# Performance work log

Hardware: AMD Instinct MI355X
Metric: run time of the kernel (lower is better)

The kernel has to match this reference:

```python
import jax, jax.numpy as jnp
import numpy as np

N = 100000
F_IN = 128
HIDDEN = 64
HEADS = 4
EPS = 1e-16
SLOPE = 0.2  # PyG GATConv default negative_slope


def gat_conv(x, src, dst, W, a_src, a_dst, b, heads, out_ch, concat, n_nodes):
    # x: [N, F]; W: [F, heads*out_ch]; a_src/a_dst: [heads, out_ch]
    h = (x @ W).reshape(n_nodes, heads, out_ch)              # [N, H, C]
    alpha_s = jnp.einsum('nhc,hc->nh', h, a_src)             # [N, H]
    alpha_d = jnp.einsum('nhc,hc->nh', h, a_dst)             # [N, H]
    e = alpha_s[src] + alpha_d[dst]                          # [E, H]
    e = jnp.where(e > 0, e, SLOPE * e)                       # leaky_relu
    # segment softmax over destination node
    m = jax.ops.segment_max(e, dst, num_segments=n_nodes)    # [N, H]
    m = jnp.where(jnp.isfinite(m), m, 0.0)                   # empty segments
    ex = jnp.exp(e - m[dst])                                 # [E, H]
    denom = jax.ops.segment_sum(ex, dst, num_segments=n_nodes)  # [N, H]
    alpha = ex / (denom[dst] + EPS)                          # [E, H]
    # weighted scatter-aggregate of source features at destinations
    msg = h[src] * alpha[:, :, None]                         # [E, H, C]
    out = jax.ops.segment_sum(msg, dst, num_segments=n_nodes)  # [N, H, C]
    if concat:
        out = out.reshape(n_nodes, heads * out_ch)
    else:
        out = out.mean(axis=1)
    return out + b


def setup_inputs() -> dict:
    key = jax.random.key(0)
    ks = jax.random.split(key, 12)
    x = jax.random.normal(ks[0], (N, F_IN), dtype=jnp.float32)
    edge_index = jax.random.randint(ks[1], (2, 1600000), 0, N, dtype=jnp.int64)
    s1 = 1.0 / np.sqrt(F_IN)
    s2 = 1.0 / np.sqrt(HIDDEN)
    return {
        'x': x,
        'edge_index': edge_index,
        'W1': jax.random.normal(ks[2], (F_IN, HIDDEN), dtype=jnp.float32) * s1,
        'a_src1': jax.random.normal(ks[3], (HEADS, HIDDEN // HEADS), dtype=jnp.float32) * s2,
        'a_dst1': jax.random.normal(ks[4], (HEADS, HIDDEN // HEADS), dtype=jnp.float32) * s2,
        'b1': jnp.zeros((HIDDEN,), dtype=jnp.float32),
        'W2': jax.random.normal(ks[5], (HIDDEN, HIDDEN), dtype=jnp.float32) * s2,
        'a_src2': jax.random.normal(ks[6], (1, HIDDEN), dtype=jnp.float32) * s2,
        'a_dst2': jax.random.normal(ks[7], (1, HIDDEN), dtype=jnp.float32) * s2,
        'b2': jnp.zeros((HIDDEN,), dtype=jnp.float32),
        'Wc': jax.random.normal(ks[8], (HIDDEN, 1), dtype=jnp.float32) * s2,
        'bc': jnp.zeros((1,), dtype=jnp.float32),
    }


def reference(x, edge_index, W1, a_src1, a_dst1, b1, W2, a_src2, a_dst2, b2, Wc, bc):
    src, dst = edge_index[0], edge_index[1]
    # dropout layers are identity in eval mode
    h = gat_conv(x, src, dst, W1, a_src1, a_dst1, b1,
                 heads=HEADS, out_ch=HIDDEN // HEADS, concat=True, n_nodes=N)
    h = jax.nn.relu(h)
    h = gat_conv(h, src, dst, W2, a_src2, a_dst2, b2,
                 heads=1, out_ch=HIDDEN, concat=False, n_nodes=N)
    h = jax.nn.relu(h)
    return h @ Wc + bc  # [N, 1]
```

## Files before the change

kernel.cpp:

```cpp
#include <hip/hip_runtime.h>
#include <hip/hip_bf16.h>


typedef __hip_bfloat16 bf16;
typedef unsigned short ushort;
typedef unsigned char uchar;
typedef __attribute__((ext_vector_type(8))) short short8;
typedef __attribute__((ext_vector_type(4))) float f32x4;

#define NN 100000
#define EE 1600000
#define BKB 9
#define BKN (1 << BKB)
#define NBK ((NN + BKN - 1) >> BKB)
#define CAP 10240
#define TILE 4096
#define EPT 16
#define NT ((EE + TILE - 1) / TILE)
#define BN 16
#define CHE 512

__device__ __forceinline__ float relu_np(float v) { return (v < 0.f) ? 0.f : v; }
__device__ __forceinline__ float lrelu(float v) { return v > 0.f ? v : 0.2f * v; }
__device__ __forceinline__ ushort f2bf(float f) {
    __hip_bfloat16 h = __float2bfloat16(f);
    return *reinterpret_cast<ushort*>(&h);
}
__device__ __forceinline__ float bf2f(ushort u) {
    unsigned int x = ((unsigned int)u) << 16;
    return __uint_as_float(x);
}

__global__ __launch_bounds__(256) void k_init(
    int* __restrict__ gcur, const float* __restrict__ W2,
    const float* __restrict__ aS2, const float* __restrict__ aD2,
    ushort* __restrict__ wExt)
{
    const int tid = threadIdx.x;
    if (tid < NBK) gcur[tid] = tid * CAP;
    for (int i = tid; i < 80 * 64; i += 256) {
        int n = i >> 6, k = i & 63;
        float v = 0.f;
        if (n < 64) {
            v = W2[k * 64 + n];
        } else if (n == 64) {
            for (int c = 0; c < 64; ++c) v = fmaf(W2[k * 64 + c], aS2[c], v);
        } else if (n == 65) {
            for (int c = 0; c < 64; ++c) v = fmaf(W2[k * 64 + c], aD2[c], v);
        }
        wExt[i] = f2bf(v);
    }
}

__global__ __launch_bounds__(256) void k_part(
    const int* __restrict__ src, const int* __restrict__ dst,
    int* __restrict__ gcur, int* __restrict__ pairs, int E)
{
    __shared__ int lh[NBK];
    __shared__ int lbase[NBK];
    const int tid = threadIdx.x;
    for (int i = tid; i < NBK; i += 256) lh[i] = 0;
    __syncthreads();
    const int e0 = blockIdx.x * TILE;
    int pk[EPT], bk[EPT], rv[EPT];
    #pragma unroll
    for (int j = 0; j < EPT; ++j) {
        int e = e0 + j * 256 + tid;
        if (e < E) {
            int d = dst[e];
            bk[j] = d >> BKB;
            pk[j] = src[e] | ((d & (BKN - 1)) << 17);
            rv[j] = atomicAdd(&lh[bk[j]], 1);
        }
    }
    __syncthreads();
    for (int i = tid; i < NBK; i += 256)
        lbase[i] = lh[i] ? atomicAdd(&gcur[i], lh[i]) : 0;
    __syncthreads();
    #pragma unroll
    for (int j = 0; j < EPT; ++j) {
        int e = e0 + j * 256 + tid;
        if (e < E) pairs[lbase[bk[j]] + rv[j]] = pk[j];
    }
}

__global__ __launch_bounds__(256) void k_bucket(
    const int* __restrict__ gcur, const int* __restrict__ pairs,
    int* __restrict__ row_ptr, uchar* __restrict__ rcnt,
    int* __restrict__ col, int N)
{
    __shared__ int hist[BKN];
    __shared__ int sP[256];
    const int b = blockIdx.x;
    const int n0 = b << BKB;
    const int tid = threadIdx.x;
    const int base = b * CAP, endE = gcur[b];
    for (int i = tid; i < BKN; i += 256) hist[i] = 0;
    __syncthreads();
    for (int i = base + tid; i < endE; i += 256)
        atomicAdd(&hist[pairs[i] >> 17], 1);
    __syncthreads();
    int a0 = hist[2 * tid], a1 = hist[2 * tid + 1];
    int tot = a0 + a1;
    sP[tid] = tot;
    __syncthreads();
    for (int off = 1; off < 256; off <<= 1) {
        int t = (tid >= off) ? sP[tid - off] : 0;
        __syncthreads();
        sP[tid] += t;
        __syncthreads();
    }
    const int excl = sP[tid] - tot;
    const int c0 = base + excl;
    hist[2 * tid] = c0;
    hist[2 * tid + 1] = c0 + a0;
    if (n0 + 2 * tid < N) {
        row_ptr[n0 + 2 * tid] = c0;
        rcnt[n0 + 2 * tid] = (uchar)a0;
    }
    if (n0 + 2 * tid + 1 < N) {
        row_ptr[n0 + 2 * tid + 1] = c0 + a0;
        rcnt[n0 + 2 * tid + 1] = (uchar)a1;
    }
    __syncthreads();
    for (int i = base + tid; i < endE; i += 256) {
        int pr = pairs[i];
        int p = atomicAdd(&hist[pr >> 17], 1);
        col[p] = pr & 0x1FFFF;
    }
}

__global__ __launch_bounds__(256) void k_gemm1(
    const float* __restrict__ x, const float* __restrict__ W1,
    const float* __restrict__ aS, const float* __restrict__ aD,
    ushort* __restrict__ h1, float* __restrict__ as1, float* __restrict__ ad1,
    int N)
{
    __shared__ ushort wB[64 * 128];
    __shared__ ushort wE[16 * 128];
    const int tid = threadIdx.x;
    for (int i = tid; i < 128 * 64; i += 256) {
        int k = i >> 6, n = i & 63;
        wB[n * 128 + k] = f2bf(W1[i]);
    }
    for (int i = tid; i < 128 * 16; i += 256) {
        int k = i >> 4, j = i & 15;
        float v = 0.f;
        if (j < 8) {
            int h = j & 3;
            const float* av = (j < 4) ? aS : aD;
            for (int c = 0; c < 16; ++c)
                v = fmaf(W1[k * 64 + h * 16 + c], av[h * 16 + c], v);
        }
        wE[j * 128 + k] = f2bf(v);
    }
    __syncthreads();
    const int w = tid >> 6, lane = tid & 63;
    const int m = lane & 15, quad = lane >> 4;
    const int ntiles = N >> 4;
    for (int tile = blockIdx.x * 4 + w; tile < ntiles; tile += gridDim.x * 4) {
        const int row0 = tile << 4;
        f32x4 acc[4] = {f32x4{0,0,0,0}, f32x4{0,0,0,0},
                        f32x4{0,0,0,0}, f32x4{0,0,0,0}};
        f32x4 acc5 = {0, 0, 0, 0};
        const float* xp = x + (size_t)(row0 + m) * 128 + quad * 8;
        #pragma unroll
        for (int ks = 0; ks < 128; ks += 32) {
            f32x4 x0 = *(const f32x4*)(xp + ks);
            f32x4 x1 = *(const f32x4*)(xp + ks + 4);
            short8 a;
            #pragma unroll
            for (int j = 0; j < 4; ++j) a[j] = (short)f2bf(x0[j]);
            #pragma unroll
            for (int j = 0; j < 4; ++j) a[4 + j] = (short)f2bf(x1[j]);
            #pragma unroll
            for (int t = 0; t < 4; ++t) {
                short8 b = *(const short8*)&wB[(t * 16 + m) * 128 + ks + quad * 8];
                acc[t] = __builtin_amdgcn_mfma_f32_16x16x32_bf16(a, b, acc[t], 0, 0, 0);
            }
            short8 b5 = *(const short8*)&wE[m * 128 + ks + quad * 8];
            acc5 = __builtin_amdgcn_mfma_f32_16x16x32_bf16(a, b5, acc5, 0, 0, 0);
        }
        #pragma unroll
        for (int t = 0; t < 4; ++t)
            #pragma unroll
            for (int r = 0; r < 4; ++r)
                h1[(size_t)(row0 + quad * 4 + r) * 64 + t * 16 + m] = f2bf(acc[t][r]);
        #pragma unroll
        for (int r = 0; r < 4; ++r) {
            int row = row0 + quad * 4 + r;
            if (m < 4) as1[row * 4 + m] = acc5[r];
            else if (m < 8) ad1[row * 4 + (m - 4)] = acc5[r];
        }
    }
}

__global__ __launch_bounds__(256, 8) void k_seg1f(
    const int* __restrict__ rp, const uchar* __restrict__ rcnt,
    const int* __restrict__ col,
    const float* __restrict__ as1, const float* __restrict__ ad1,
    const ushort* __restrict__ h1, const float* __restrict__ b1,
    const ushort* __restrict__ wExt,
    ushort* __restrict__ h2, float* __restrict__ as2, float* __restrict__ ad2,
    int N)
{
    __shared__ __align__(16) ushort zS[BN * 72];
    __shared__ float pS[CHE * 4];
    __shared__ int colS[CHE];
    __shared__ uchar ndS[CHE];
    __shared__ int sRp[BN + 1];
    __shared__ float bS[64];
    __shared__ float adS[BN * 4];

    const int tid = threadIdx.x;
    const int n0 = blockIdx.x * BN;

    if (tid < 64) bS[tid] = b1[tid];
    if (tid < BN * 4) adS[tid] = ad1[(size_t)n0 * 4 + tid];
    if (tid < BN) sRp[tid] = rp[n0 + tid];
    if (tid == BN) sRp[BN] = rp[n0 + BN - 1] + (int)rcnt[n0 + BN - 1];
    __syncthreads();

    const int eb0 = sRp[0];
    const int cnt = min(sRp[BN] - eb0, CHE);

    for (int t = tid; t < cnt; t += 256) {
        int ge = eb0 + t;
        colS[t] = col[ge];
        int nd = 0;
        #pragma unroll
        for (int k = 1; k < BN; ++k) nd += (ge >= sRp[k]);
        ndS[t] = (uchar)nd;
    }
    __syncthreads();
    for (int t = tid; t < cnt * 4; t += 256) {
        int e = t >> 2, hh = t & 3;
        float v = as1[(size_t)colS[e] * 4 + hh] + adS[ndS[e] * 4 + hh];
        pS[t] = __expf(lrelu(v));
    }
    __syncthreads();

    const int w = tid >> 6, lane = tid & 63;
    const int slot = lane >> 4, c4 = lane & 15, head = c4 >> 2;
    const int uid = slot * 4 + (c4 & 3);

    for (int nl = 0; nl < 4; ++nl) {
        const int nb = w * 4 + nl;
        const int s_n = sRp[nb] - eb0, e_n = sRp[nb + 1] - eb0;
        float den = 0.f;
        f32x4 accA = {0,0,0,0}, accB = {0,0,0,0};
        for (int i = s_n + uid; i < e_n; i += 16) den += pS[i * 4 + head];
        int i = s_n;
        for (; i + 7 < e_n; i += 8) {
            int lA = i + slot, lB = lA + 4;
            float pA = pS[lA * 4 + head], pB = pS[lB * 4 + head];
            ushort4 hA = *(const ushort4*)&h1[(size_t)colS[lA] * 64 + c4 * 4];
            ushort4 hB = *(const ushort4*)&h1[(size_t)colS[lB] * 64 + c4 * 4];
            accA[0] = fmaf(pA, bf2f(hA.x), accA[0]);
            accA[1] = fmaf(pA, bf2f(hA.y), accA[1]);
            accA[2] = fmaf(pA, bf2f(hA.z), accA[2]);
            accA[3] = fmaf(pA, bf2f(hA.w), accA[3]);
            accB[0] = fmaf(pB, bf2f(hB.x), accB[0]);
            accB[1] = fmaf(pB, bf2f(hB.y), accB[1]);
            accB[2] = fmaf(pB, bf2f(hB.z), accB[2]);
            accB[3] = fmaf(pB, bf2f(hB.w), accB[3]);
        }
        for (; i < e_n; i += 4) {
            int ii = i + slot;
            if (ii < e_n) {
                float p = pS[ii * 4 + head];
                ushort4 hv = *(const ushort4*)&h1[(size_t)colS[ii] * 64 + c4 * 4];
                accA[0] = fmaf(p, bf2f(hv.x), accA[0]);
                accA[1] = fmaf(p, bf2f(hv.y), accA[1]);
                accA[2] = fmaf(p, bf2f(hv.z), accA[2]);
                accA[3] = fmaf(p, bf2f(hv.w), accA[3]);
            }
        }
        den += __shfl_xor(den, 1);
        den += __shfl_xor(den, 2);
        den += __shfl_xor(den, 16);
        den += __shfl_xor(den, 32);
        #pragma unroll
        for (int j = 0; j < 4; ++j) {
            accA[j] += accB[j];
            accA[j] += __shfl_xor(accA[j], 16);
            accA[j] += __shfl_xor(accA[j], 32);
        }
        if (slot == 0) {
            float inv = 1.f / (den + 1e-16f);
            ushort4 zv;
            zv.x = f2bf(relu_np(accA[0] * inv + bS[c4 * 4 + 0]));
            zv.y = f2bf(relu_np(accA[1] * inv + bS[c4 * 4 + 1]));
            zv.z = f2bf(relu_np(accA[2] * inv + bS[c4 * 4 + 2]));
            zv.w = f2bf(relu_np(accA[3] * inv + bS[c4 * 4 + 3]));
            *(ushort4*)&zS[nb * 72 + c4 * 4] = zv;
        }
    }
    __syncthreads();

    const int m = c4, quad = slot;
    for (int t = w; t < 5; t += 4) {
        f32x4 acc = {0, 0, 0, 0};
        #pragma unroll
        for (int ks = 0; ks < 64; ks += 32) {
            short8 a = *(const short8*)&zS[m * 72 + ks + quad * 8];
            short8 b = *(const short8*)&wExt[(t * 16 + m) * 64 + ks + quad * 8];
            acc = __builtin_amdgcn_mfma_f32_16x16x32_bf16(a, b, acc, 0, 0, 0);
        }
        if (t < 4) {
            #pragma unroll
            for (int r = 0; r < 4; ++r)
                h2[(size_t)(n0 + quad * 4 + r) * 64 + t * 16 + m] = f2bf(acc[r]);
        } else {
            #pragma unroll
            for (int r = 0; r < 4; ++r) {
                int row = n0 + quad * 4 + r;
                if (m == 0) as2[row] = acc[r];
                else if (m == 1) ad2[row] = acc[r];
            }
        }
    }
}

__global__ __launch_bounds__(256, 8) void k_seg2f(
    const int* __restrict__ rp, const uchar* __restrict__ rcnt,
    const int* __restrict__ col,
    const float* __restrict__ as2, const float* __restrict__ ad2,
    const ushort* __restrict__ h2, const float* __restrict__ b2,
    const float* __restrict__ Wc, const float* __restrict__ bc,
    float* __restrict__ out, int N)
{
    __shared__ float pS[CHE];
    __shared__ int colS[CHE];
    __shared__ uchar ndS[CHE];
    __shared__ int sRp[BN + 1];
    __shared__ float adS[BN];
    __shared__ float b2S[64];
    __shared__ float wcS[64];

    const int tid = threadIdx.x;
    const int n0 = blockIdx.x * BN;
    if (tid < 64) { b2S[tid] = b2[tid]; wcS[tid] = Wc[tid]; }
    if (tid < BN) { sRp[tid] = rp[n0 + tid]; adS[tid] = ad2[n0 + tid]; }
    if (tid == BN) sRp[BN] = rp[n0 + BN - 1] + (int)rcnt[n0 + BN - 1];
    __syncthreads();

    const int eb0 = sRp[0];
    const int cnt = min(sRp[BN] - eb0, CHE);
    for (int t = tid; t < cnt; t += 256) {
        int ge = eb0 + t;
        colS[t] = col[ge];
        int nd = 0;
        #pragma unroll
        for (int k = 1; k < BN; ++k) nd += (ge >= sRp[k]);
        ndS[t] = (uchar)nd;
    }
    __syncthreads();
    for (int t = tid; t < cnt; t += 256)
        pS[t] = __expf(lrelu(as2[colS[t]] + adS[ndS[t]]));
    __syncthreads();

    const int w = tid >> 6, lane = tid & 63;
    const int slot = lane >> 4, c4 = lane & 15;

    for (int nl = 0; nl < 4; ++nl) {
        const int nb = w * 4 + nl;
        const int myn = n0 + nb;
        const int s_n = sRp[nb] - eb0, e_n = sRp[nb + 1] - eb0;
        float den = 0.f;
        f32x4 accA = {0,0,0,0}, accB = {0,0,0,0};
        for (int i = s_n + lane; i < e_n; i += 64) den += pS[i];
        int i = s_n;
        for (; i + 7 < e_n; i += 8) {
            int lA = i + slot, lB = lA + 4;
            float pA = pS[lA], pB = pS[lB];
            ushort4 hA = *(const ushort4*)&h2[(size_t)colS[lA] * 64 + c4 * 4];
            ushort4 hB = *(const ushort4*)&h2[(size_t)colS[lB] * 64 + c4 * 4];
            accA[0] = fmaf(pA, bf2f(hA.x), accA[0]);
            accA[1] = fmaf(pA, bf2f(hA.y), accA[1]);
            accA[2] = fmaf(pA, bf2f(hA.z), accA[2]);
            accA[3] = fmaf(pA, bf2f(hA.w), accA[3]);
            accB[0] = fmaf(pB, bf2f(hB.x), accB[0]);
            accB[1] = fmaf(pB, bf2f(hB.y), accB[1]);
            accB[2] = fmaf(pB, bf2f(hB.z), accB[2]);
            accB[3] = fmaf(pB, bf2f(hB.w), accB[3]);
        }
        for (; i < e_n; i += 4) {
            int ii = i + slot;
            if (ii < e_n) {
                float p = pS[ii];
                ushort4 hv = *(const ushort4*)&h2[(size_t)colS[ii] * 64 + c4 * 4];
                accA[0] = fmaf(p, bf2f(hv.x), accA[0]);
                accA[1] = fmaf(p, bf2f(hv.y), accA[1]);
                accA[2] = fmaf(p, bf2f(hv.z), accA[2]);
                accA[3] = fmaf(p, bf2f(hv.w), accA[3]);
            }
        }
        #pragma unroll
        for (int off = 32; off >= 1; off >>= 1) den += __shfl_xor(den, off);
        #pragma unroll
        for (int j = 0; j < 4; ++j) {
            accA[j] += accB[j];
            accA[j] += __shfl_xor(accA[j], 16);
            accA[j] += __shfl_xor(accA[j], 32);
        }
        if (slot == 0) {
            float inv = 1.f / (den + 1e-16f);
            float t2 = 0.f;
            #pragma unroll
            for (int j = 0; j < 4; ++j)
                t2 += relu_np(accA[j] * inv + b2S[c4 * 4 + j]) * wcS[c4 * 4 + j];
            t2 += __shfl_xor(t2, 1);
            t2 += __shfl_xor(t2, 2);
            t2 += __shfl_xor(t2, 4);
            t2 += __shfl_xor(t2, 8);
            if (c4 == 0) out[myn] = t2 + bc[0];
        }
    }
}

extern "C" void kernel_launch(void* const* d_in, const int* in_sizes, int n_in,
                              void* d_out, int out_size, void* d_ws, size_t ws_size,
                              hipStream_t stream)
{
    const float* x   = (const float*)d_in[0];
    const int*   ei  = (const int*)d_in[1];
    const float* W1  = (const float*)d_in[2];
    const float* aS1 = (const float*)d_in[3];
    const float* aD1 = (const float*)d_in[4];
    const float* b1  = (const float*)d_in[5];
    const float* W2  = (const float*)d_in[6];
    const float* aS2 = (const float*)d_in[7];
    const float* aD2 = (const float*)d_in[8];
    const float* b2  = (const float*)d_in[9];
    const float* Wc  = (const float*)d_in[10];
    const float* bc  = (const float*)d_in[11];
    float* out = (float*)d_out;

    const int N = NN;
    const int E = EE;
    const int* src = ei;
    const int* dst = ei + E;

    ushort* h1   = (ushort*)d_ws;
    ushort* h2   = h1 + (size_t)N * 64;
    float*  as1  = (float*)(h2 + (size_t)N * 64);
    float*  ad1  = as1 + (size_t)N * 4;
    float*  as2  = ad1 + (size_t)N * 4;
    float*  ad2  = as2 + (size_t)N;
    ushort* wExt = (ushort*)(ad2 + (size_t)N);
    int* row_ptr = (int*)(wExt + 80 * 64);
    uchar* rcnt  = (uchar*)(row_ptr + N);
    int* gcur    = (int*)(rcnt + ((N + 3) & ~3));
    int* col     = gcur + NBK;
    int* pairs   = (int*)h2;

    k_init<<<1, 256, 0, stream>>>(gcur, W2, aS2, aD2, wExt);
    k_part<<<NT, 256, 0, stream>>>(src, dst, gcur, pairs, E);
    k_bucket<<<NBK, 256, 0, stream>>>(gcur, pairs, row_ptr, rcnt, col, N);

    k_gemm1<<<782, 256, 0, stream>>>(x, W1, aS1, aD1, h1, as1, ad1, N);

    k_seg1f<<<N / BN, 256, 0, stream>>>(row_ptr, rcnt, col, as1, ad1, h1, b1,
                                        wExt, h2, as2, ad2, N);

    k_seg2f<<<N / BN, 256, 0, stream>>>(row_ptr, rcnt, col, as2, ad2, h2,
                                        b2, Wc, bc, out, N);
}
```

Before: 284.5 us.

## Assign one 16-lane group per node in GAT aggregation instead of per-warp node loop

Both aggregation kernels change how work is mapped to lanes. Before, each wave looped over 4 nodes, spreading each node's edges across 4 slots with cross-slot shuffle reductions. Now each 16-lane group owns one node, walks all of its edges serially with 4-way unrolled gathers, and accumulates the denominator inline. This removes the separate denominator pass and the cross-slot shuffle reductions, and keeps all 4 nodes in flight at once. In exchange, each lane runs a longer serial loop per node, and lanes whose nodes have skewed degrees may sit idle.

Result: faster. 267.8 us (-5.8%).

```diff
diff --git a/kernel.cpp b/kernel.cpp
--- a/kernel.cpp
+++ b/kernel.cpp
@@ -241,82 +241,79 @@
     __syncthreads();
 
     const int w = tid >> 6, lane = tid & 63;
-    const int slot = lane >> 4, c4 = lane & 15, head = c4 >> 2;
-    const int uid = slot * 4 + (c4 & 3);
-
-    for (int nl = 0; nl < 4; ++nl) {
-        const int nb = w * 4 + nl;
-        const int s_n = sRp[nb] - eb0, e_n = sRp[nb + 1] - eb0;
-        float den = 0.f;
-        f32x4 accA = {0,0,0,0}, accB = {0,0,0,0};
-        for (int i = s_n + uid; i < e_n; i += 16) den += pS[i * 4 + head];
-        int i = s_n;
-        for (; i + 7 < e_n; i += 8) {
-            int lA = i + slot, lB = lA + 4;
-            float pA = pS[lA * 4 + head], pB = pS[lB * 4 + head];
-            ushort4 hA = *(const ushort4*)&h1[(size_t)colS[lA] * 64 + c4 * 4];
-            ushort4 hB = *(const ushort4*)&h1[(size_t)colS[lB] * 64 + c4 * 4];
-            accA[0] = fmaf(pA, bf2f(hA.x), accA[0]);
-            accA[1] = fmaf(pA, bf2f(hA.y), accA[1]);
-            accA[2] = fmaf(pA, bf2f(hA.z), accA[2]);
-            accA[3] = fmaf(pA, bf2f(hA.w), accA[3]);
-            accB[0] = fmaf(pB, bf2f(hB.x), accB[0]);
-            accB[1] = fmaf(pB, bf2f(hB.y), accB[1]);
-            accB[2] = fmaf(pB, bf2f(hB.z), accB[2]);
-            accB[3] = fmaf(pB, bf2f(hB.w), accB[3]);
-        }
-        for (; i < e_n; i += 4) {
-            int ii = i + slot;
-            if (ii < e_n) {
-                float p = pS[ii * 4 + head];
-                ushort4 hv = *(const ushort4*)&h1[(size_t)colS[ii] * 64 + c4 * 4];
-                accA[0] = fmaf(p, bf2f(hv.x), accA[0]);
-                accA[1] = fmaf(p, bf2f(hv.y), accA[1]);
-                accA[2] = fmaf(p, bf2f(hv.z), accA[2]);
-                accA[3] = fmaf(p, bf2f(hv.w), accA[3]);
-            }
-        }
-        den += __shfl_xor(den, 1);
-        den += __shfl_xor(den, 2);
-        den += __shfl_xor(den, 16);
-        den += __shfl_xor(den, 32);
-        #pragma unroll
-        for (int j = 0; j < 4; ++j) {
-            accA[j] += accB[j];
-            accA[j] += __shfl_xor(accA[j], 16);
-            accA[j] += __shfl_xor(accA[j], 32);
-        }
-        if (slot == 0) {
-            float inv = 1.f / (den + 1e-16f);
-            ushort4 zv;
-            zv.x = f2bf(relu_np(accA[0] * inv + bS[c4 * 4 + 0]));
-            zv.y = f2bf(relu_np(accA[1] * inv + bS[c4 * 4 + 1]));
-            zv.z = f2bf(relu_np(accA[2] * inv + bS[c4 * 4 + 2]));
-            zv.w = f2bf(relu_np(accA[3] * inv + bS[c4 * 4 + 3]));
-            *(ushort4*)&zS[nb * 72 + c4 * 4] = zv;
-        }
-    }
-    __syncthreads();
-
-    const int m = c4, quad = slot;
+    const int g = lane >> 4, c4 = lane & 15, head = c4 >> 2;
+    const int nb = w * 4 + g;
+    const int s_n = sRp[nb] - eb0, e_n = sRp[nb + 1] - eb0;
+
+    f32x4 acc = {0, 0, 0, 0};
+    float den = 0.f;
+    int i = s_n;
+    for (; i + 3 < e_n; i += 4) {
+        int cA = colS[i], cB = colS[i + 1], cC = colS[i + 2], cD = colS[i + 3];
+        ushort4 hA = *(const ushort4*)&h1[(size_t)cA * 64 + c4 * 4];
+        ushort4 hB = *(const ushort4*)&h1[(size_t)cB * 64 + c4 * 4];
+        ushort4 hC = *(const ushort4*)&h1[(size_t)cC * 64 + c4 * 4];
+        ushort4 hD = *(const ushort4*)&h1[(size_t)cD * 64 + c4 * 4];
+        float pA = pS[(i + 0) * 4 + head], pB = pS[(i + 1) * 4 + head];
+        float pC = pS[(i + 2) * 4 + head], pD = pS[(i + 3) * 4 + head];
+        den += (pA + pB) + (pC + pD);
+        acc[0] = fmaf(pA, bf2f(hA.x), acc[0]);
+        acc[1] = fmaf(pA, bf2f(hA.y), acc[1]);
+        acc[2] = fmaf(pA, bf2f(hA.z), acc[2]);
+        acc[3] = fmaf(pA, bf2f(hA.w), acc[3]);
+        acc[0] = fmaf(pB, bf2f(hB.x), acc[0]);
+        acc[1] = fmaf(pB, bf2f(hB.y), acc[1]);
+        acc[2] = fmaf(pB, bf2f(hB.z), acc[2]);
+        acc[3] = fmaf(pB, bf2f(hB.w), acc[3]);
+        acc[0] = fmaf(pC, bf2f(hC.x), acc[0]);
+        acc[1] = fmaf(pC, bf2f(hC.y), acc[1]);
+        acc[2] = fmaf(pC, bf2f(hC.z), acc[2]);
+        acc[3] = fmaf(pC, bf2f(hC.w), acc[3]);
+        acc[0] = fmaf(pD, bf2f(hD.x), acc[0]);
+        acc[1] = fmaf(pD, bf2f(hD.y), acc[1]);
+        acc[2] = fmaf(pD, bf2f(hD.z), acc[2]);
+        acc[3] = fmaf(pD, bf2f(hD.w), acc[3]);
+    }
+    for (; i < e_n; ++i) {
+        int cA = colS[i];
+        ushort4 hA = *(const ushort4*)&h1[(size_t)cA * 64 + c4 * 4];
+        float pA = pS[i * 4 + head];
+        den += pA;
+        acc[0] = fmaf(pA, bf2f(hA.x), acc[0]);
+        acc[1] = fmaf(pA, bf2f(hA.y), acc[1]);
+        acc[2] = fmaf(pA, bf2f(hA.z), acc[2]);
+        acc[3] = fmaf(pA, bf2f(hA.w), acc[3]);
+    }
+    {
+        float inv = 1.f / (den + 1e-16f);
+        ushort4 zv;
+        zv.x = f2bf(relu_np(acc[0] * inv + bS[c4 * 4 + 0]));
+        zv.y = f2bf(relu_np(acc[1] * inv + bS[c4 * 4 + 1]));
+        zv.z = f2bf(relu_np(acc[2] * inv + bS[c4 * 4 + 2]));
+        zv.w = f2bf(relu_np(acc[3] * inv + bS[c4 * 4 + 3]));
+        *(ushort4*)&zS[nb * 72 + c4 * 4] = zv;
+    }
+    __syncthreads();
+
+    const int m = c4, quad = g;
     for (int t = w; t < 5; t += 4) {
-        f32x4 acc = {0, 0, 0, 0};
+        f32x4 acct = {0, 0, 0, 0};
         #pragma unroll
         for (int ks = 0; ks < 64; ks += 32) {
             short8 a = *(const short8*)&zS[m * 72 + ks + quad * 8];
             short8 b = *(const short8*)&wExt[(t * 16 + m) * 64 + ks + quad * 8];
-            acc = __builtin_amdgcn_mfma_f32_16x16x32_bf16(a, b, acc, 0, 0, 0);
+            acct = __builtin_amdgcn_mfma_f32_16x16x32_bf16(a, b, acct, 0, 0, 0);
         }
         if (t < 4) {
             #pragma unroll
             for (int r = 0; r < 4; ++r)
-                h2[(size_t)(n0 + quad * 4 + r) * 64 + t * 16 + m] = f2bf(acc[r]);
+                h2[(size_t)(n0 + quad * 4 + r) * 64 + t * 16 + m] = f2bf(acct[r]);
         } else {
             #pragma unroll
             for (int r = 0; r < 4; ++r) {
                 int row = n0 + quad * 4 + r;
-                if (m == 0) as2[row] = acc[r];
-                else if (m == 1) ad2[row] = acc[r];
+                if (m == 0) as2[row] = acct[r];
+                else if (m == 1) ad2[row] = acct[r];
             }
         }
     }
@@ -361,62 +358,60 @@
     __syncthreads();
 
     const int w = tid >> 6, lane = tid & 63;
-    const int slot = lane >> 4, c4 = lane & 15;
-
-    for (int nl = 0; nl < 4; ++nl) {
-        const int nb = w * 4 + nl;
-        const int myn = n0 + nb;
-        const int s_n = sRp[nb] - eb0, e_n = sRp[nb + 1] - eb0;
-        float den = 0.f;
-        f32x4 accA = {0,0,0,0}, accB = {0,0,0,0};
-        for (int i = s_n + lane; i < e_n; i += 64) den += pS[i];
-        int i = s_n;
-        for (; i + 7 < e_n; i += 8) {
-            int lA = i + slot, lB = lA + 4;
-            float pA = pS[lA], pB = pS[lB];
-            ushort4 hA = *(const ushort4*)&h2[(size_t)colS[lA] * 64 + c4 * 4];
-            ushort4 hB = *(const ushort4*)&h2[(size_t)colS[lB] * 64 + c4 * 4];
-            accA[0] = fmaf(pA, bf2f(hA.x), accA[0]);
-            accA[1] = fmaf(pA, bf2f(hA.y), accA[1]);
-            accA[2] = fmaf(pA, bf2f(hA.z), accA[2]);
-            accA[3] = fmaf(pA, bf2f(hA.w), accA[3]);
-            accB[0] = fmaf(pB, bf2f(hB.x), accB[0]);
-            accB[1] = fmaf(pB, bf2f(hB.y), accB[1]);
-            accB[2] = fmaf(pB, bf2f(hB.z), accB[2]);
-            accB[3] = fmaf(pB, bf2f(hB.w), accB[3]);
-        }
-        for (; i < e_n; i += 4) {
-            int ii = i + slot;
-            if (ii < e_n) {
-                float p = pS[ii];
-                ushort4 hv = *(const ushort4*)&h2[(size_t)colS[ii] * 64 + c4 * 4];
-                accA[0] = fmaf(p, bf2f(hv.x), accA[0]);
-                accA[1] = fmaf(p, bf2f(hv.y), accA[1]);
-                accA[2] = fmaf(p, bf2f(hv.z), accA[2]);
-                accA[3] = fmaf(p, bf2f(hv.w), accA[3]);
-            }
-        }
-        #pragma unroll
-        for (int off = 32; off >= 1; off >>= 1) den += __shfl_xor(den, off);
-        #pragma unroll
-        for (int j = 0; j < 4; ++j) {
-            accA[j] += accB[j];
-            accA[j] += __shfl_xor(accA[j], 16);
-            accA[j] += __shfl_xor(accA[j], 32);
-        }
-        if (slot == 0) {
-            float inv = 1.f / (den + 1e-16f);
-            float t2 = 0.f;
-            #pragma unroll
-            for (int j = 0; j < 4; ++j)
-                t2 += relu_np(accA[j] * inv + b2S[c4 * 4 + j]) * wcS[c4 * 4 + j];
-            t2 += __shfl_xor(t2, 1);
-            t2 += __shfl_xor(t2, 2);
-            t2 += __shfl_xor(t2, 4);
-            t2 += __shfl_xor(t2, 8);
-            if (c4 == 0) out[myn] = t2 + bc[0];
-        }
-    }
+    const int g = lane >> 4, c4 = lane & 15;
+    const int nb = w * 4 + g;
+    const int myn = n0 + nb;
+    const int s_n = sRp[nb] - eb0, e_n = sRp[nb + 1] - eb0;
+
+    f32x4 acc = {0, 0, 0, 0};
+    float den = 0.f;
+    int i = s_n;
+    for (; i + 3 < e_n; i += 4) {
+        int cA = colS[i], cB = colS[i + 1], cC = colS[i + 2], cD = colS[i + 3];
+        ushort4 hA = *(const ushort4*)&h2[(size_t)cA * 64 + c4 * 4];
+        ushort4 hB = *(const ushort4*)&h2[(size_t)cB * 64 + c4 * 4];
+        ushort4 hC = *(const ushort4*)&h2[(size_t)cC * 64 + c4 * 4];
+        ushort4 hD = *(const ushort4*)&h2[(size_t)cD * 64 + c4 * 4];
+        float pA = pS[i + 0], pB = pS[i + 1], pC = pS[i + 2], pD = pS[i + 3];
+        den += (pA + pB) + (pC + pD);
+        acc[0] = fmaf(pA, bf2f(hA.x), acc[0]);
+        acc[1] = fmaf(pA, bf2f(hA.y), acc[1]);
+        acc[2] = fmaf(pA, bf2f(hA.z), acc[2]);
+        acc[3] = fmaf(pA, bf2f(hA.w), acc[3]);
+        acc[0] = fmaf(pB, bf2f(hB.x), acc[0]);
+        acc[1] = fmaf(pB, bf2f(hB.y), acc[1]);
+        acc[2] = fmaf(pB, bf2f(hB.z), acc[2]);
+        acc[3] = fmaf(pB, bf2f(hB.w), acc[3]);
+        acc[0] = fmaf(pC, bf2f(hC.x), acc[0]);
+        acc[1] = fmaf(pC, bf2f(hC.y), acc[1]);
+        acc[2] = fmaf(pC, bf2f(hC.z), acc[2]);
+        acc[3] = fmaf(pC, bf2f(hC.w), acc[3]);
+        acc[0] = fmaf(pD, bf2f(hD.x), acc[0]);
+        acc[1] = fmaf(pD, bf2f(hD.y), acc[1]);
+        acc[2] = fmaf(pD, bf2f(hD.z), acc[2]);
+        acc[3] = fmaf(pD, bf2f(hD.w), acc[3]);
+    }
+    for (; i < e_n; ++i) {
+        int cA = colS[i];
+        ushort4 hA = *(const ushort4*)&h2[(size_t)cA * 64 + c4 * 4];
+        float pA = pS[i];
+        den += pA;
+        acc[0] = fmaf(pA, bf2f(hA.x), acc[0]);
+        acc[1] = fmaf(pA, bf2f(hA.y), acc[1]);
+        acc[2] = fmaf(pA, bf2f(hA.z), acc[2]);
+        acc[3] = fmaf(pA, bf2f(hA.w), acc[3]);
+    }
+
+    float inv = 1.f / (den + 1e-16f);
+    float t2 = 0.f;
+    #pragma unroll
+    for (int j = 0; j < 4; ++j)
+        t2 += relu_np(acc[j] * inv + b2S[c4 * 4 + j]) * wcS[c4 * 4 + j];
+    t2 += __shfl_xor(t2, 1);
+    t2 += __shfl_xor(t2, 2);
+    t2 += __shfl_xor(t2, 4);
+    t2 += __shfl_xor(t2, 8);
+    if (c4 == 0) out[myn] = t2 + bc[0];
 }
 
 extern "C" void kernel_launch(void* const* d_in, const int* in_sizes, int n_in,
```
